# Performance work log

Measured on AMD Instinct MI355X. Metric: run time of the kernel, lower is better.

## Reference

```python
import jax, jax.numpy as jnp
import numpy as np

K = 20  # kNN fan-out


def knn_idx(x, k):
    # x: (B, C, N). Negative squared pairwise distance; top-k largest = nearest.
    inner = -2.0 * jnp.einsum('bcn,bcm->bnm', x, x)        # (B, N, N)
    xx = jnp.sum(x * x, axis=1)                            # (B, N)
    pd = -xx[:, :, None] - inner - xx[:, None, :]          # (B, N, N)
    return jax.lax.top_k(pd, k)[1]                         # (B, N, k) int32


def get_graph_feature(x, k):
    # x: (B, C, N) -> edge features (B, 2C, N, k)
    idx = knn_idx(x, k)                                    # (B, N, k)
    xt = jnp.transpose(x, (0, 2, 1))                       # (B, N, C)
    nbrs = jax.vmap(lambda pts, ids: pts[ids])(xt, idx)    # (B, N, k, C)
    center = xt[:, :, None, :]                             # (B, N, 1, C)
    feat = jnp.concatenate(
        [nbrs - center, jnp.broadcast_to(center, nbrs.shape)], axis=-1)  # (B,N,k,2C)
    return jnp.transpose(feat, (0, 3, 1, 2))               # (B, 2C, N, k)


def vn_layer(W, x):
    # W: (out, in); x: (B, in, N, k) -> (B, out, N, k)
    return jnp.einsum('oi,bink->bonk', W, x)


def setup_inputs() -> dict:
    key = jax.random.key(0)
    ks = jax.random.split(key, 6)
    B, C, N = 16, 3, 2048
    num_classes = 10
    return {
        'x': jax.random.normal(ks[0], (B, C, N), dtype=jnp.float32),
        'W1': jax.random.normal(ks[1], (64, 6), dtype=jnp.float32),
        'W2': jax.random.normal(ks[2], (128, 64), dtype=jnp.float32),
        'W3': jax.random.normal(ks[3], (256, 128), dtype=jnp.float32),
        'fc_w': jax.random.normal(ks[4], (num_classes, 256), dtype=jnp.float32) * 0.0625,
        'fc_b': jax.random.normal(ks[5], (num_classes,), dtype=jnp.float32) * 0.0625,
    }


def reference(x, W1, W2, W3, fc_w, fc_b):
    h = get_graph_feature(x, K)          # (B, 6, N, k)
    h = vn_layer(W1, h)                  # (B, 64, N, k)
    h = jax.nn.relu(vn_layer(W2, h))     # (B, 128, N, k)
    h = jax.nn.relu(vn_layer(W3, h))     # (B, 256, N, k)
    h = jnp.max(h, axis=-1)              # max over neighbors k -> (B, 256, N)
    h = jnp.max(h, axis=-1)              # global max over points -> (B, 256)
    return h @ fc_w.T + fc_b             # (B, num_classes)
```

## Files before the change

### kernel.cpp

```cpp
#include <hip/hip_runtime.h>
#include <stdint.h>

typedef _Float16 v8h __attribute__((ext_vector_type(8)));
typedef _Float16 v2h __attribute__((ext_vector_type(2)));
typedef float v4f __attribute__((ext_vector_type(4)));
typedef float v16f __attribute__((ext_vector_type(16)));

#define NPTS 2048
#define BATCH 16
#define KNN 20
#define PAIRS (NPTS * KNN)

__device__ __forceinline__ unsigned pair_relu_h2(unsigned pu, unsigned qu) {
  v2h a = *(const v2h*)&pu;
  v2h b = *(const v2h*)&qu;
  v2h s = a + b;
  v2h z = {(_Float16)0.f, (_Float16)0.f};
  v2h r = __builtin_elementwise_max(s, z);
  return *(const unsigned*)&r;
}
__device__ __forceinline__ float fmax3(float a, float b, float c) {
  return fmaxf(fmaxf(a, b), c);
}

__global__ __launch_bounds__(512, 2) void knn_kernel(
    const float* __restrict__ x, int* __restrict__ idxOut,
    const float* __restrict__ W1, const float* __restrict__ W2,
    unsigned short* __restrict__ p, unsigned short* __restrict__ q,
    int* __restrict__ H) {
  __shared__ float4 pts[NPTS];
  __shared__ unsigned long long cand[8][8][64];
  __shared__ float M2s[128][6];
  int b = blockIdx.x >> 5;
  int qblk = blockIdx.x & 31;
  const float* xb = x + b * 3 * NPTS;

  if (qblk == 0 && threadIdx.x < 256) H[b * 256 + threadIdx.x] = 0;

  for (int i = threadIdx.x; i < NPTS; i += 512) {
    float X = xb[i], Y = xb[NPTS + i], Z = xb[2 * NPTS + i];
    pts[i] = make_float4(X, Y, Z, X * X + Y * Y + Z * Z);
  }

  if (threadIdx.x < 128) {
    int o = threadIdx.x;
    const float* w2 = W2 + o * 64;
    float a0 = 0, a1 = 0, a2 = 0, a3 = 0, a4 = 0, a5 = 0;
    for (int i = 0; i < 64; ++i) {
      const float* w1r = W1 + i * 6;
      float w = w2[i];
      a0 += w * w1r[0]; a1 += w * w1r[1]; a2 += w * w1r[2];
      a3 += w * (w1r[3] - w1r[0]); a4 += w * (w1r[4] - w1r[1]); a5 += w * (w1r[5] - w1r[2]);
    }
    M2s[o][0] = a0; M2s[o][1] = a1; M2s[o][2] = a2;
    M2s[o][3] = a3; M2s[o][4] = a4; M2s[o][5] = a5;
  }
  __syncthreads();

  int wid = threadIdx.x >> 6, lane = threadIdx.x & 63;
  int qbase = qblk * 64 + wid * 8;

  {
    int o0 = lane * 2;
    float a0 = M2s[o0][0], a1 = M2s[o0][1], a2 = M2s[o0][2];
    float a3 = M2s[o0][3], a4 = M2s[o0][4], a5 = M2s[o0][5];
    float c0 = M2s[o0 + 1][0], c1 = M2s[o0 + 1][1], c2 = M2s[o0 + 1][2];
    float c3 = M2s[o0 + 1][3], c4 = M2s[o0 + 1][4], c5 = M2s[o0 + 1][5];
    unsigned* pw = (unsigned*)p;
    unsigned* qw = (unsigned*)q;
#pragma unroll
    for (int g = 0; g < 8; ++g) {
      int j = qbase + g;
      float4 qp = pts[j];
      float p0 = a0 * qp.x + a1 * qp.y + a2 * qp.z;
      float p1 = c0 * qp.x + c1 * qp.y + c2 * qp.z;
      float q0 = a3 * qp.x + a4 * qp.y + a5 * qp.z;
      float q1 = c3 * qp.x + c4 * qp.y + c5 * qp.z;
      size_t base = ((size_t)(b * NPTS + j)) * 64 + lane;
      auto hp = __builtin_amdgcn_cvt_pkrtz(p0, p1);
      auto hq = __builtin_amdgcn_cvt_pkrtz(q0, q1);
      pw[base] = *(const unsigned*)&hp;
      qw[base] = *(const unsigned*)&hq;
    }
  }

  float m2x[8], m2y[8], m2z[8], mn[8];
#pragma unroll
  for (int g = 0; g < 8; ++g) {
    float4 qp = pts[qbase + g];
    m2x[g] = -2.f * qp.x; m2y[g] = -2.f * qp.y; m2z[g] = -2.f * qp.z;
    mn[g] = 1e30f;
  }

  for (int s = 0; s < 32; ++s) {
    float4 P = pts[s * 64 + lane];
#pragma unroll
    for (int g = 0; g < 8; ++g) {
      float d = fmaf(m2x[g], P.x, fmaf(m2y[g], P.y, fmaf(m2z[g], P.z, P.w)));
      mn[g] = fminf(mn[g], d);
    }
  }

  float tau[8];
#pragma unroll
  for (int g = 0; g < 8; ++g) {
    float v = mn[g];
    for (int k = 2; k <= 64; k <<= 1) {
      for (int j = k >> 1; j > 0; j >>= 1) {
        float o = __shfl_xor(v, j);
        bool low = (lane & j) == 0;
        bool up = (lane & k) == 0;
        v = (low == up) ? fminf(v, o) : fmaxf(v, o);
      }
    }
    float t = __shfl(v, 19);
    tau[g] = t + fabsf(t) * 4e-6f + 1e-6f;
  }

  int cnt[8] = {0, 0, 0, 0, 0, 0, 0, 0};
  for (int s = 0; s < 32; ++s) {
    int i = s * 64 + lane;
    float4 P = pts[i];
#pragma unroll
    for (int g = 0; g < 8; ++g) {
      float d = fmaf(m2x[g], P.x, fmaf(m2y[g], P.y, fmaf(m2z[g], P.z, P.w)));
      bool take = d <= tau[g];
      unsigned long long mb = __ballot(take);
      if (take) {
        int pos = cnt[g] + __popcll(mb & ((1ull << lane) - 1ull));
        if (pos < 64) {
          unsigned kd = __float_as_uint(d + 64.f);
          cand[wid][g][pos] = (((unsigned long long)kd) << 32) | (unsigned)i;
        }
      }
      cnt[g] += __popcll(mb);
    }
  }

#pragma unroll
  for (int g = 0; g < 8; ++g) {
    int nc = cnt[g] < 64 ? cnt[g] : 64;
    unsigned long long k0 = (lane < nc) ? cand[wid][g][lane] : ~0ull;
    int r0 = 0;
    for (int i = 0; i < nc; ++i) r0 += (cand[wid][g][i] < k0) ? 1 : 0;
    long long obase = ((long long)b * NPTS + qbase + g) * KNN;
    if (lane < nc && r0 < KNN) idxOut[obase + r0] = (int)(k0 & 0xffffffffu);
  }
}

__global__ __launch_bounds__(256, 3) void gemm_max_kernel(
    const unsigned short* __restrict__ p, const unsigned short* __restrict__ q,
    const int* __restrict__ idx, const float* __restrict__ W3, int* __restrict__ H) {
  __shared__ __align__(16) unsigned short h2s[2][2][32 * 128];

  int b = blockIdx.x & 15;
  int w = blockIdx.x >> 4;
  int t = threadIdx.x;
  int lane = t & 63, wid = t >> 6;
  int col = lane & 31, hi = lane >> 5;

  v8h bfr0[8], bfr1[8];
#pragma unroll
  for (int kk = 0; kk < 8; ++kk) {
    const float* s0 = W3 + (size_t)(wid * 64 + col) * 128 + kk * 16 + hi * 8;
    const float* s1 = s0 + 32 * 128;
    v8h f0, f1;
#pragma unroll
    for (int jj = 0; jj < 8; ++jj) { f0[jj] = (_Float16)s0[jj]; f1[jj] = (_Float16)s1[jj]; }
    bfr0[kk] = f0; bfr1[kk] = f1;
  }

  const unsigned short* pB = p + (size_t)b * NPTS * 128;
  const unsigned short* qB = q + (size_t)b * NPTS * 128;
  const int* idxB = idx + (size_t)b * PAIRS;

  int pm = t >> 3;
  int c2 = t & 7;
  int st0 = pm * 128 + (((c2 * 2) ^ (pm & 7)) * 8);
  int st1 = pm * 128 + (((c2 * 2 + 1) ^ (pm & 7)) * 8);

  const int NT = PAIRS / 32;

  uint4 PA0, PA1, QA0, QA1, PB0, PB1, QB0, QB1;
  int jnA, jnB;
  {
    int prA = w * 32 + pm, prB = (w + 64) * 32 + pm;
    int jA = idxB[prA] & (NPTS - 1);
    int jB = idxB[prB] & (NPTS - 1);
    int nA = prA / 20, nB = prB / 20;
    PA0 = *(const uint4*)(pB + (size_t)jA * 128 + c2 * 16);
    PA1 = *(const uint4*)(pB + (size_t)jA * 128 + c2 * 16 + 8);
    QA0 = *(const uint4*)(qB + (size_t)nA * 128 + c2 * 16);
    QA1 = *(const uint4*)(qB + (size_t)nA * 128 + c2 * 16 + 8);
    PB0 = *(const uint4*)(pB + (size_t)jB * 128 + c2 * 16);
    PB1 = *(const uint4*)(pB + (size_t)jB * 128 + c2 * 16 + 8);
    QB0 = *(const uint4*)(qB + (size_t)nB * 128 + c2 * 16);
    QB1 = *(const uint4*)(qB + (size_t)nB * 128 + c2 * 16 + 8);
    jnA = idxB[(w + 128) * 32 + pm];
    jnB = idxB[(w + 192) * 32 + pm];
  }

  float vmx0 = 0.f, vmx1 = 0.f;
  int buf = 0;
  for (int T = w; T < NT; T += 128) {
    uint4 R;
    R.x = pair_relu_h2(PA0.x, QA0.x); R.y = pair_relu_h2(PA0.y, QA0.y);
    R.z = pair_relu_h2(PA0.z, QA0.z); R.w = pair_relu_h2(PA0.w, QA0.w);
    *(uint4*)&h2s[buf][0][st0] = R;
    R.x = pair_relu_h2(PA1.x, QA1.x); R.y = pair_relu_h2(PA1.y, QA1.y);
    R.z = pair_relu_h2(PA1.z, QA1.z); R.w = pair_relu_h2(PA1.w, QA1.w);
    *(uint4*)&h2s[buf][0][st1] = R;
    R.x = pair_relu_h2(PB0.x, QB0.x); R.y = pair_relu_h2(PB0.y, QB0.y);
    R.z = pair_relu_h2(PB0.z, QB0.z); R.w = pair_relu_h2(PB0.w, QB0.w);
    *(uint4*)&h2s[buf][1][st0] = R;
    R.x = pair_relu_h2(PB1.x, QB1.x); R.y = pair_relu_h2(PB1.y, QB1.y);
    R.z = pair_relu_h2(PB1.z, QB1.z); R.w = pair_relu_h2(PB1.w, QB1.w);
    *(uint4*)&h2s[buf][1][st1] = R;
    __syncthreads();

    int Tn = T + 128;
    if (Tn < NT) {
      int prA = Tn * 32 + pm, prB = (Tn + 64) * 32 + pm;
      int jA = jnA & (NPTS - 1), jB = jnB & (NPTS - 1);
      int nA = prA / 20, nB = prB / 20;
      PA0 = *(const uint4*)(pB + (size_t)jA * 128 + c2 * 16);
      PA1 = *(const uint4*)(pB + (size_t)jA * 128 + c2 * 16 + 8);
      QA0 = *(const uint4*)(qB + (size_t)nA * 128 + c2 * 16);
      QA1 = *(const uint4*)(qB + (size_t)nA * 128 + c2 * 16 + 8);
      PB0 = *(const uint4*)(pB + (size_t)jB * 128 + c2 * 16);
      PB1 = *(const uint4*)(pB + (size_t)jB * 128 + c2 * 16 + 8);
      QB0 = *(const uint4*)(qB + (size_t)nB * 128 + c2 * 16);
      QB1 = *(const uint4*)(qB + (size_t)nB * 128 + c2 * 16 + 8);
      int T2 = T + 256;
      if (T2 < NT) {
        jnA = idxB[T2 * 32 + pm];
        jnB = idxB[(T2 + 64) * 32 + pm];
      }
    }

    {
      v16f acc0 = {0.f}, acc1 = {0.f};
#pragma unroll
      for (int kk = 0; kk < 8; ++kk) {
        v8h a = *(const v8h*)&h2s[buf][0][col * 128 + (((kk * 2 + hi) ^ (col & 7)) * 8)];
        acc0 = __builtin_amdgcn_mfma_f32_32x32x16_f16(a, bfr0[kk], acc0, 0, 0, 0);
        acc1 = __builtin_amdgcn_mfma_f32_32x32x16_f16(a, bfr1[kk], acc1, 0, 0, 0);
      }
      float m0 = fmax3(acc0[0], acc0[1], acc0[2]);
      float m1 = fmax3(acc0[3], acc0[4], acc0[5]);
      float m2 = fmax3(acc0[6], acc0[7], acc0[8]);
      float m3 = fmax3(acc0[9], acc0[10], acc0[11]);
      float m4 = fmax3(acc0[12], acc0[13], acc0[14]);
      vmx0 = fmax3(fmax3(m0, m1, m2), fmax3(m3, m4, acc0[15]), vmx0);
      float n0 = fmax3(acc1[0], acc1[1], acc1[2]);
      float n1 = fmax3(acc1[3], acc1[4], acc1[5]);
      float n2 = fmax3(acc1[6], acc1[7], acc1[8]);
      float n3 = fmax3(acc1[9], acc1[10], acc1[11]);
      float n4 = fmax3(acc1[12], acc1[13], acc1[14]);
      vmx1 = fmax3(fmax3(n0, n1, n2), fmax3(n3, n4, acc1[15]), vmx1);
    }
    {
      v16f acc0 = {0.f}, acc1 = {0.f};
#pragma unroll
      for (int kk = 0; kk < 8; ++kk) {
        v8h a = *(const v8h*)&h2s[buf][1][col * 128 + (((kk * 2 + hi) ^ (col & 7)) * 8)];
        acc0 = __builtin_amdgcn_mfma_f32_32x32x16_f16(a, bfr0[kk], acc0, 0, 0, 0);
        acc1 = __builtin_amdgcn_mfma_f32_32x32x16_f16(a, bfr1[kk], acc1, 0, 0, 0);
      }
      float m0 = fmax3(acc0[0], acc0[1], acc0[2]);
      float m1 = fmax3(acc0[3], acc0[4], acc0[5]);
      float m2 = fmax3(acc0[6], acc0[7], acc0[8]);
      float m3 = fmax3(acc0[9], acc0[10], acc0[11]);
      float m4 = fmax3(acc0[12], acc0[13], acc0[14]);
      vmx0 = fmax3(fmax3(m0, m1, m2), fmax3(m3, m4, acc0[15]), vmx0);
      float n0 = fmax3(acc1[0], acc1[1], acc1[2]);
      float n1 = fmax3(acc1[3], acc1[4], acc1[5]);
      float n2 = fmax3(acc1[6], acc1[7], acc1[8]);
      float n3 = fmax3(acc1[9], acc1[10], acc1[11]);
      float n4 = fmax3(acc1[12], acc1[13], acc1[14]);
      vmx1 = fmax3(fmax3(n0, n1, n2), fmax3(n3, n4, acc1[15]), vmx1);
    }
    buf ^= 1;
  }

  float v0 = fmaxf(vmx0, __shfl_xor(vmx0, 32));
  float v1 = fmaxf(vmx1, __shfl_xor(vmx1, 32));
  if (hi == 0) {
    atomicMax(&H[b * 256 + wid * 64 + col], __float_as_int(v0));
    atomicMax(&H[b * 256 + wid * 64 + 32 + col], __float_as_int(v1));
  }
}

__global__ __launch_bounds__(64) void fc_kernel(const int* __restrict__ Hi,
                                                const float* __restrict__ fcw,
                                                const float* __restrict__ fcb,
                                                float* __restrict__ out) {
  int b = blockIdx.x / 10, r = blockIdx.x % 10;
  int lane = threadIdx.x;
  const float* Hb = (const float*)Hi + b * 256;
  float s = 0.f;
#pragma unroll
  for (int c = lane; c < 256; c += 64) s += Hb[c] * fcw[r * 256 + c];
#pragma unroll
  for (int m = 32; m > 0; m >>= 1) s += __shfl_xor(s, m);
  if (lane == 0) out[b * 10 + r] = s + fcb[r];
}

extern "C" void kernel_launch(void* const* d_in, const int* in_sizes, int n_in,
                              void* d_out, int out_size, void* d_ws, size_t ws_size,
                              hipStream_t stream) {
  const float* x   = (const float*)d_in[0];
  const float* W1  = (const float*)d_in[1];
  const float* W2  = (const float*)d_in[2];
  const float* W3  = (const float*)d_in[3];
  const float* fcw = (const float*)d_in[4];
  const float* fcb = (const float*)d_in[5];
  float* out = (float*)d_out;
  char* ws = (char*)d_ws;

  int* H     = (int*)(ws + 4096);
  int* idx   = (int*)(ws + 24576);
  unsigned short* p = (unsigned short*)(ws + 3145728);
  unsigned short* q = (unsigned short*)(ws + 12582912);

  knn_kernel<<<BATCH * 32, 512, 0, stream>>>(x, idx, W1, W2, p, q, H);
  gemm_max_kernel<<<BATCH * 64, 256, 0, stream>>>(p, q, idx, W3, H);
  fc_kernel<<<BATCH * 10, 64, 0, stream>>>(H, fcw, fcb, out);
}
```

Before: 158.0 us.

## Warp-specialize gemm_max into producer/consumer waves with LDS ring buffer

```diff
diff --git a/kernel.cpp b/kernel.cpp
--- a/kernel.cpp
+++ b/kernel.cpp
@@ -148,104 +148,116 @@
   }
 }
 
-__global__ __launch_bounds__(256, 3) void gemm_max_kernel(
+__global__ __launch_bounds__(384) void gemm_max_kernel(
     const unsigned short* __restrict__ p, const unsigned short* __restrict__ q,
     const int* __restrict__ idx, const float* __restrict__ W3, int* __restrict__ H) {
-  __shared__ __align__(16) unsigned short h2s[2][2][32 * 128];
+#define RING 6
+#define NTIL 40
+  __shared__ __align__(16) unsigned short tile[RING][32 * 128];
+  __shared__ int ready0[RING], ready1[RING], used[RING];
 
   int b = blockIdx.x & 15;
   int w = blockIdx.x >> 4;
   int t = threadIdx.x;
-  int lane = t & 63, wid = t >> 6;
-  int col = lane & 31, hi = lane >> 5;
-
-  v8h bfr0[8], bfr1[8];
-#pragma unroll
-  for (int kk = 0; kk < 8; ++kk) {
-    const float* s0 = W3 + (size_t)(wid * 64 + col) * 128 + kk * 16 + hi * 8;
-    const float* s1 = s0 + 32 * 128;
-    v8h f0, f1;
-#pragma unroll
-    for (int jj = 0; jj < 8; ++jj) { f0[jj] = (_Float16)s0[jj]; f1[jj] = (_Float16)s1[jj]; }
-    bfr0[kk] = f0; bfr1[kk] = f1;
-  }
+  int wid = t >> 6, lane = t & 63;
+
+  if (t < RING) { ready0[t] = -1; ready1[t] = -1; used[t] = 0; }
+  __syncthreads();
 
   const unsigned short* pB = p + (size_t)b * NPTS * 128;
   const unsigned short* qB = q + (size_t)b * NPTS * 128;
   const int* idxB = idx + (size_t)b * PAIRS;
 
-  int pm = t >> 3;
-  int c2 = t & 7;
-  int st0 = pm * 128 + (((c2 * 2) ^ (pm & 7)) * 8);
-  int st1 = pm * 128 + (((c2 * 2 + 1) ^ (pm & 7)) * 8);
-
-  const int NT = PAIRS / 32;
-
-  uint4 PA0, PA1, QA0, QA1, PB0, PB1, QB0, QB1;
-  int jnA, jnB;
-  {
-    int prA = w * 32 + pm, prB = (w + 64) * 32 + pm;
-    int jA = idxB[prA] & (NPTS - 1);
-    int jB = idxB[prB] & (NPTS - 1);
-    int nA = prA / 20, nB = prB / 20;
-    PA0 = *(const uint4*)(pB + (size_t)jA * 128 + c2 * 16);
-    PA1 = *(const uint4*)(pB + (size_t)jA * 128 + c2 * 16 + 8);
-    QA0 = *(const uint4*)(qB + (size_t)nA * 128 + c2 * 16);
-    QA1 = *(const uint4*)(qB + (size_t)nA * 128 + c2 * 16 + 8);
-    PB0 = *(const uint4*)(pB + (size_t)jB * 128 + c2 * 16);
-    PB1 = *(const uint4*)(pB + (size_t)jB * 128 + c2 * 16 + 8);
-    QB0 = *(const uint4*)(qB + (size_t)nB * 128 + c2 * 16);
-    QB1 = *(const uint4*)(qB + (size_t)nB * 128 + c2 * 16 + 8);
-    jnA = idxB[(w + 128) * 32 + pm];
-    jnB = idxB[(w + 192) * 32 + pm];
-  }
-
-  float vmx0 = 0.f, vmx1 = 0.f;
-  int buf = 0;
-  for (int T = w; T < NT; T += 128) {
-    uint4 R;
-    R.x = pair_relu_h2(PA0.x, QA0.x); R.y = pair_relu_h2(PA0.y, QA0.y);
-    R.z = pair_relu_h2(PA0.z, QA0.z); R.w = pair_relu_h2(PA0.w, QA0.w);
-    *(uint4*)&h2s[buf][0][st0] = R;
-    R.x = pair_relu_h2(PA1.x, QA1.x); R.y = pair_relu_h2(PA1.y, QA1.y);
-    R.z = pair_relu_h2(PA1.z, QA1.z); R.w = pair_relu_h2(PA1.w, QA1.w);
-    *(uint4*)&h2s[buf][0][st1] = R;
-    R.x = pair_relu_h2(PB0.x, QB0.x); R.y = pair_relu_h2(PB0.y, QB0.y);
-    R.z = pair_relu_h2(PB0.z, QB0.z); R.w = pair_relu_h2(PB0.w, QB0.w);
-    *(uint4*)&h2s[buf][1][st0] = R;
-    R.x = pair_relu_h2(PB1.x, QB1.x); R.y = pair_relu_h2(PB1.y, QB1.y);
-    R.z = pair_relu_h2(PB1.z, QB1.z); R.w = pair_relu_h2(PB1.w, QB1.w);
-    *(uint4*)&h2s[buf][1][st1] = R;
-    __syncthreads();
-
-    int Tn = T + 128;
-    if (Tn < NT) {
-      int prA = Tn * 32 + pm, prB = (Tn + 64) * 32 + pm;
-      int jA = jnA & (NPTS - 1), jB = jnB & (NPTS - 1);
-      int nA = prA / 20, nB = prB / 20;
-      PA0 = *(const uint4*)(pB + (size_t)jA * 128 + c2 * 16);
-      PA1 = *(const uint4*)(pB + (size_t)jA * 128 + c2 * 16 + 8);
-      QA0 = *(const uint4*)(qB + (size_t)nA * 128 + c2 * 16);
-      QA1 = *(const uint4*)(qB + (size_t)nA * 128 + c2 * 16 + 8);
-      PB0 = *(const uint4*)(pB + (size_t)jB * 128 + c2 * 16);
-      PB1 = *(const uint4*)(pB + (size_t)jB * 128 + c2 * 16 + 8);
-      QB0 = *(const uint4*)(qB + (size_t)nB * 128 + c2 * 16);
-      QB1 = *(const uint4*)(qB + (size_t)nB * 128 + c2 * 16 + 8);
-      int T2 = T + 256;
-      if (T2 < NT) {
-        jnA = idxB[T2 * 32 + pm];
-        jnB = idxB[(T2 + 64) * 32 + pm];
-      }
-    }
-
-    {
+  if (wid < 2) {
+    int plane = wid * 64 + lane;
+    int pair = plane >> 2;
+    int quarter = plane & 3;
+    int stoff[4];
+#pragma unroll
+    for (int k = 0; k < 4; ++k)
+      stoff[k] = pair * 128 + (((quarter * 4 + k) ^ (pair & 7)) * 8);
+
+    uint4 P[2][4], Q[2][4];
+#pragma unroll
+    for (int s0 = 0; s0 < 2; ++s0) {
+      int pr = (w + s0 * 32) * 32 + pair;
+      int j = idxB[pr] & (NPTS - 1);
+      unsigned n = (unsigned)pr / 20u;
+#pragma unroll
+      for (int k = 0; k < 4; ++k) {
+        P[s0][k] = *(const uint4*)(pB + (size_t)j * 128 + quarter * 32 + k * 8);
+        Q[s0][k] = *(const uint4*)(qB + (size_t)n * 128 + quarter * 32 + k * 8);
+      }
+    }
+    for (int s = 0; s < NTIL; ++s) {
+      int slot = s - (s / RING) * RING;
+      int e = s / RING;
+      if (e > 0) {
+        while (__hip_atomic_load(&used[slot], __ATOMIC_ACQUIRE,
+                                 __HIP_MEMORY_SCOPE_WORKGROUP) < 4 * e)
+          __builtin_amdgcn_s_sleep(2);
+      }
+      int d = s & 1;
+#pragma unroll
+      for (int k = 0; k < 4; ++k) {
+        uint4 R;
+        R.x = pair_relu_h2(P[d][k].x, Q[d][k].x);
+        R.y = pair_relu_h2(P[d][k].y, Q[d][k].y);
+        R.z = pair_relu_h2(P[d][k].z, Q[d][k].z);
+        R.w = pair_relu_h2(P[d][k].w, Q[d][k].w);
+        *(uint4*)&tile[slot][stoff[k]] = R;
+      }
+      if (lane == 0) {
+        if (wid == 0)
+          __hip_atomic_store(&ready0[slot], s, __ATOMIC_RELEASE, __HIP_MEMORY_SCOPE_WORKGROUP);
+        else
+          __hip_atomic_store(&ready1[slot], s, __ATOMIC_RELEASE, __HIP_MEMORY_SCOPE_WORKGROUP);
+      }
+      int sn = s + 2;
+      if (sn < NTIL) {
+        int pr = (w + sn * 32) * 32 + pair;
+        int j = idxB[pr] & (NPTS - 1);
+        unsigned n = (unsigned)pr / 20u;
+#pragma unroll
+        for (int k = 0; k < 4; ++k) {
+          P[d][k] = *(const uint4*)(pB + (size_t)j * 128 + quarter * 32 + k * 8);
+          Q[d][k] = *(const uint4*)(qB + (size_t)n * 128 + quarter * 32 + k * 8);
+        }
+      }
+    }
+  } else {
+    int cg = wid - 2;
+    int col = lane & 31, hi = lane >> 5;
+    v8h bfr0[8], bfr1[8];
+#pragma unroll
+    for (int kk = 0; kk < 8; ++kk) {
+      const float* s0 = W3 + (size_t)(cg * 64 + col) * 128 + kk * 16 + hi * 8;
+      const float* s1 = s0 + 32 * 128;
+      v8h f0, f1;
+#pragma unroll
+      for (int jj = 0; jj < 8; ++jj) { f0[jj] = (_Float16)s0[jj]; f1[jj] = (_Float16)s1[jj]; }
+      bfr0[kk] = f0; bfr1[kk] = f1;
+    }
+
+    float vmx0 = 0.f, vmx1 = 0.f;
+    for (int s = 0; s < NTIL; ++s) {
+      int slot = s - (s / RING) * RING;
+      while (__hip_atomic_load(&ready0[slot], __ATOMIC_ACQUIRE,
+                               __HIP_MEMORY_SCOPE_WORKGROUP) < s ||
+             __hip_atomic_load(&ready1[slot], __ATOMIC_ACQUIRE,
+                               __HIP_MEMORY_SCOPE_WORKGROUP) < s)
+        __builtin_amdgcn_s_sleep(2);
+
       v16f acc0 = {0.f}, acc1 = {0.f};
 #pragma unroll
       for (int kk = 0; kk < 8; ++kk) {
-        v8h a = *(const v8h*)&h2s[buf][0][col * 128 + (((kk * 2 + hi) ^ (col & 7)) * 8)];
+        v8h a = *(const v8h*)&tile[slot][col * 128 + (((kk * 2 + hi) ^ (col & 7)) * 8)];
         acc0 = __builtin_amdgcn_mfma_f32_32x32x16_f16(a, bfr0[kk], acc0, 0, 0, 0);
         acc1 = __builtin_amdgcn_mfma_f32_32x32x16_f16(a, bfr1[kk], acc1, 0, 0, 0);
       }
+      if (lane == 0)
+        __hip_atomic_fetch_add(&used[slot], 1, __ATOMIC_RELEASE, __HIP_MEMORY_SCOPE_WORKGROUP);
+
       float m0 = fmax3(acc0[0], acc0[1], acc0[2]);
       float m1 = fmax3(acc0[3], acc0[4], acc0[5]);
       float m2 = fmax3(acc0[6], acc0[7], acc0[8]);
@@ -259,36 +271,16 @@
       float n4 = fmax3(acc1[12], acc1[13], acc1[14]);
       vmx1 = fmax3(fmax3(n0, n1, n2), fmax3(n3, n4, acc1[15]), vmx1);
     }
-    {
-      v16f acc0 = {0.f}, acc1 = {0.f};
-#pragma unroll
-      for (int kk = 0; kk < 8; ++kk) {
-        v8h a = *(const v8h*)&h2s[buf][1][col * 128 + (((kk * 2 + hi) ^ (col & 7)) * 8)];
-        acc0 = __builtin_amdgcn_mfma_f32_32x32x16_f16(a, bfr0[kk], acc0, 0, 0, 0);
-        acc1 = __builtin_amdgcn_mfma_f32_32x32x16_f16(a, bfr1[kk], acc1, 0, 0, 0);
-      }
-      float m0 = fmax3(acc0[0], acc0[1], acc0[2]);
-      float m1 = fmax3(acc0[3], acc0[4], acc0[5]);
-      float m2 = fmax3(acc0[6], acc0[7], acc0[8]);
-      float m3 = fmax3(acc0[9], acc0[10], acc0[11]);
-      float m4 = fmax3(acc0[12], acc0[13], acc0[14]);
-      vmx0 = fmax3(fmax3(m0, m1, m2), fmax3(m3, m4, acc0[15]), vmx0);
-      float n0 = fmax3(acc1[0], acc1[1], acc1[2]);
-      float n1 = fmax3(acc1[3], acc1[4], acc1[5]);
-      float n2 = fmax3(acc1[6], acc1[7], acc1[8]);
-      float n3 = fmax3(acc1[9], acc1[10], acc1[11]);
-      float n4 = fmax3(acc1[12], acc1[13], acc1[14]);
-      vmx1 = fmax3(fmax3(n0, n1, n2), fmax3(n3, n4, acc1[15]), vmx1);
-    }
-    buf ^= 1;
-  }
-
-  float v0 = fmaxf(vmx0, __shfl_xor(vmx0, 32));
-  float v1 = fmaxf(vmx1, __shfl_xor(vmx1, 32));
-  if (hi == 0) {
-    atomicMax(&H[b * 256 + wid * 64 + col], __float_as_int(v0));
-    atomicMax(&H[b * 256 + wid * 64 + 32 + col], __float_as_int(v1));
-  }
+
+    float v0 = fmaxf(vmx0, __shfl_xor(vmx0, 32));
+    float v1 = fmaxf(vmx1, __shfl_xor(vmx1, 32));
+    if (hi == 0) {
+      atomicMax(&H[b * 256 + cg * 64 + col], __float_as_int(v0));
+      atomicMax(&H[b * 256 + cg * 64 + 32 + col], __float_as_int(v1));
+    }
+  }
+#undef RING
+#undef NTIL
 }
 
 __global__ __launch_bounds__(64) void fc_kernel(const int* __restrict__ Hi,
@@ -324,6 +316,6 @@
   unsigned short* q = (unsigned short*)(ws + 12582912);
 
   knn_kernel<<<BATCH * 32, 512, 0, stream>>>(x, idx, W1, W2, p, q, H);
-  gemm_max_kernel<<<BATCH * 64, 256, 0, stream>>>(p, q, idx, W3, H);
+  gemm_max_kernel<<<BATCH * 32, 384, 0, stream>>>(p, q, idx, W3, H);
   fc_kernel<<<BATCH * 10, 64, 0, stream>>>(H, fcw, fcb, out);
 }
```

Measured after the change: 226.3 us. +43.2%, slower.
